# Kernel optimization log

Measured on AMD Instinct MI355X. Metric: run time of the kernel, lower is better.

The kernel has to match this reference:

```python
import jax, jax.numpy as jnp
import numpy as np

B, U, N0, N1, E, H = 8, 8192, 64, 64, 128, 8
S = N0 * N1


def setup_inputs() -> dict:
    key = jax.random.key(0)
    ks = jax.random.split(key, 9)
    # regular grid over [-1, 1]^2 (meshgrid, 'ij' indexing)
    c0 = jnp.linspace(-1.0, 1.0, N0)
    c1 = jnp.linspace(-1.0, 1.0, N1)
    g0, g1 = jnp.meshgrid(c0, c1, indexing='ij')
    xc_on_grid = jnp.broadcast_to(jnp.stack([g0, g1], -1), (B, N0, N1, 2))
    xc_off_grid = jax.random.uniform(ks[0], (B, U, 2), minval=-1.0, maxval=1.0)
    zc_off_grid = jax.random.normal(ks[1], (B, U, E))
    zc_on_grid = jax.random.normal(ks[2], (B, N0, N1, E))
    latents = jax.random.normal(ks[3], (N0, N1, E))
    fake_embedding = jax.random.normal(ks[4], (E,))
    sc = 1.0 / np.sqrt(E).astype(np.float32)
    Wq = jax.random.normal(ks[5], (E, E)) * sc
    Wk = jax.random.normal(ks[6], (E, E)) * sc
    Wv = jax.random.normal(ks[7], (E, E)) * sc
    Wo = jax.random.normal(ks[8], (E, E)) * sc
    return dict(xc_off_grid=xc_off_grid, xc_on_grid=xc_on_grid,
                zc_off_grid=zc_off_grid, zc_on_grid=zc_on_grid,
                latents=latents, fake_embedding=fake_embedding,
                Wq=Wq, Wk=Wk, Wv=Wv, Wo=Wo, used_modality=0)


def _nearest_idx(x, x_grid):
    # nearest cell on a regular grid, flattened row-major (k=1 of nearest_gridded_neighbours)
    n0, n1 = x_grid.shape[1], x_grid.shape[2]
    c0 = x_grid[:, :, 0, 0]   # [B, n0]
    c1 = x_grid[:, 0, :, 1]   # [B, n1]
    sp0 = (c0[:, 1] - c0[:, 0])[:, None]
    sp1 = (c1[:, 1] - c1[:, 0])[:, None]
    i0 = jnp.clip(jnp.round((x[..., 0] - c0[:, :1]) / sp0), 0, n0 - 1)
    i1 = jnp.clip(jnp.round((x[..., 1] - c1[:, :1]) / sp1), 0, n1 - 1)
    return (i0 * n1 + i1).astype(jnp.int32)


def _cumcount(nearest):
    # duplicate-count within each grid cell via linear-recurrence associative scan
    # (same math as the torch complex-log scan: x_t = a_t*x_{t-1} + b_t, a=b=same-flag)
    sort_idx = jnp.argsort(nearest, axis=1, stable=True)
    ns = jnp.take_along_axis(nearest, sort_idx, axis=1)
    same = (ns == jnp.roll(ns, 1, axis=1)).astype(jnp.float32)
    same = same.at[:, 0].set(0.0)

    def combine(c1, c2):
        a1, b1 = c1
        a2, b2 = c2
        return a1 * a2, a2 * b1 + b2

    _, cc = jax.lax.associative_scan(combine, (same, same), axis=1)
    unsort = jnp.argsort(sort_idx, axis=1, stable=True)
    return jnp.take_along_axis(jnp.round(cc), unsort, axis=1).astype(jnp.int32)


def _mhca(q, kv, mask, Wq, Wk, Wv, Wo):
    # q: [N,1,E], kv: [N,P,E], mask: [N,1,P] (True = attend)
    N, P, Ed = kv.shape
    dh = Ed // H
    qh = (q @ Wq).reshape(N, 1, H, dh).transpose(0, 2, 1, 3)
    kh = (kv @ Wk).reshape(N, P, H, dh).transpose(0, 2, 1, 3)
    vh = (kv @ Wv).reshape(N, P, H, dh).transpose(0, 2, 1, 3)
    scores = jnp.einsum('nhqd,nhkd->nhqk', qh, kh) / jnp.sqrt(jnp.asarray(dh, qh.dtype))
    scores = jnp.where(mask[:, None, :, :], scores, -jnp.inf)
    attn = jax.nn.softmax(scores, axis=-1)
    out = jnp.einsum('nhqk,nhkd->nhqd', attn, vh)
    return out.transpose(0, 2, 1, 3).reshape(N, 1, Ed) @ Wo


def reference(xc_off_grid, xc_on_grid, zc_off_grid, zc_on_grid, latents,
              fake_embedding, Wq, Wk, Wv, Wo, used_modality):
    # PseudoTokenGridEncoder.forward, no-coarsening branch, used_modality=OFF_GRID
    Bb, Uu, Ee = zc_off_grid.shape
    n0, n1 = xc_on_grid.shape[1], xc_on_grid.shape[2]
    Ss = n0 * n1
    nearest = _nearest_idx(xc_off_grid, xc_on_grid)         # [B, U]
    cumcount = _cumcount(nearest)                           # [B, U]
    max_patch = int(jnp.max(cumcount)) + 2                  # data-dependent (eager)
    rows = nearest.reshape(-1) + jnp.repeat(jnp.arange(Bb) * Ss, Uu)
    cols = cumcount.reshape(-1)
    grid_stacked = jnp.zeros((Bb * Ss, max_patch, Ee), zc_off_grid.dtype)
    grid_stacked = grid_stacked.at[rows, cols].set(zc_off_grid.reshape(Bb * Uu, Ee))
    grid_stacked = grid_stacked.at[:, -1].set(fake_embedding)  # OFF_GRID -> fake token
    valid = jnp.zeros((Bb * Ss, max_patch), bool)
    valid = valid.at[rows, cols].set(True).at[:, -1].set(True)
    latent_flat = jnp.broadcast_to(latents.reshape(1, Ss, Ee), (Bb, Ss, Ee)).reshape(Bb * Ss, 1, Ee)
    out = _mhca(latent_flat, grid_stacked, valid[:, None, :], Wq, Wk, Wv, Wo)
    z_grid = out.reshape(Bb, n0, n1, Ee)
    return xc_on_grid, z_grid
```

## Files before the change

### kernel.cpp

```cpp
#include <hip/hip_runtime.h>
#include <hip/hip_bf16.h>

#define NB 8
#define NU 8192
#define GN0 64
#define GN1 64
#define NS 4096
#define NE 128
#define NH 8
#define CAP 20
#define NPTS (NB * NU)
#define NCELL (NB * NS)
#define OUT0 (NB * GN0 * GN1 * 2)


typedef __attribute__((ext_vector_type(8))) short short8v;
typedef __attribute__((ext_vector_type(4))) float float4v;

static __device__ inline unsigned pk2(float a, float b) {
  __hip_bfloat16 x = __float2bfloat16(a), y = __float2bfloat16(b);
  return ((unsigned)*(unsigned short*)&y << 16) | *(unsigned short*)&x;
}
static __device__ inline float bfs(short v) {
  unsigned u = (unsigned)(unsigned short)v << 16;
  return __builtin_bit_cast(float, u);
}

__global__ __launch_bounds__(256) void setup_kernel(
    const float* __restrict__ xc_on, const float* __restrict__ fake,
    const float* __restrict__ Wk, const float* __restrict__ Wv,
    const float* __restrict__ Wo,
    float* __restrict__ out, int* __restrict__ counts,
    float* __restrict__ fakeKV, __hip_bfloat16* __restrict__ Wt,
    __hip_bfloat16* __restrict__ Wot) {
  int t = threadIdx.x;
  int blk = blockIdx.x;
  if (blk < 64) {
    int idx = blk * 256 + t;
    ((float4*)out)[idx] = ((const float4*)xc_on)[idx];
    if (idx < NCELL / 4) ((int4*)counts)[idx] = int4{0, 0, 0, 0};
    return;
  }
  if (blk == 64) {
    __shared__ float frow[NE];
    if (t < NE) frow[t] = fake[t];
    __syncthreads();
    int e = t & 127, half = t >> 7;
    const float* W = half ? Wv : Wk;
    float acc = 0.f;
    for (int j = 0; j < NE; ++j) acc += frow[j] * W[j * NE + e];
    fakeKV[half * NE + e] = acc;
    return;
  }
  {
    int flat = (blk - 65) * 256 + t;
    int j = flat >> 7, e = flat & 127;
    Wt[e * NE + j] = __float2bfloat16(Wv[flat]);
    Wt[(128 + e) * NE + j] = __float2bfloat16(Wk[flat]);
    Wot[e * NE + j] = __float2bfloat16(Wo[flat]);
  }
}

__global__ __launch_bounds__(256) void vgemm_qf_kernel(
    const float* __restrict__ z, const float* __restrict__ xc_off,
    const float* __restrict__ xc_on, const __hip_bfloat16* __restrict__ Wt,
    const float* __restrict__ latents, const float* __restrict__ Wq,
    int* __restrict__ counts, unsigned short* __restrict__ lists,
    __hip_bfloat16* __restrict__ Vb, __hip_bfloat16* __restrict__ Kb,
    float* __restrict__ qf) {
  __shared__ __hip_bfloat16 zb[64 * 136];
  int tid = threadIdx.x;
  if ((int)blockIdx.x >= 1024) {
    float* lrow = (float*)zb;
    int s0 = ((int)blockIdx.x - 1024) * 8;
    for (int i = tid; i < 8 * NE; i += 256)
      lrow[i] = latents[(size_t)s0 * NE + i];
    __syncthreads();
    for (int i = tid; i < 8 * NE; i += 256) {
      int sl = i >> 7, e = i & 127;
      float acc = 0.f;
      for (int j = 0; j < NE; ++j) acc += lrow[sl * NE + j] * Wq[j * NE + e];
      qf[(size_t)(s0 + sl) * NE + e] = acc;
    }
    return;
  }
  int blk = ((int)blockIdx.x & 7) * 128 + ((int)blockIdx.x >> 3);
  size_t row0 = (size_t)blk * 64;
  for (int n = 0; n < 8; ++n) {
    int flat = n * 1024 + tid * 4;
    int r = flat >> 7, c = flat & 127;
    float4 v = *(const float4*)&z[(row0 + r) * NE + c];
    uint2 u = {pk2(v.x, v.y), pk2(v.z, v.w)};
    *(uint2*)&zb[r * 136 + c] = u;
  }
  if (tid < 64) {
    int p = (int)row0 + tid;
    int b = p >> 13;
    const float* g = xc_on + (size_t)b * (GN0 * GN1 * 2);
    float c00 = g[0], c01 = g[GN1 * 2], c10 = g[1], c11 = g[3];
    float x0 = xc_off[(size_t)p * 2 + 0];
    float x1 = xc_off[(size_t)p * 2 + 1];
    float f0 = rintf((x0 - c00) / (c01 - c00));
    float f1 = rintf((x1 - c10) / (c11 - c10));
    int i0 = (int)fminf(fmaxf(f0, 0.f), 63.f);
    int i1 = (int)fminf(fmaxf(f1, 0.f), 63.f);
    int cell = b * NS + i0 * GN1 + i1;
    int pos = atomicAdd(&counts[cell], 1);
    if (pos < CAP) lists[cell * CAP + pos] = (unsigned short)p;
  }
  __syncthreads();
  int wid = tid >> 6, l = tid & 63;
  int lr = l & 15, lk = l >> 4;
  const short* zl = (const short*)zb;
  const short* Wg = (const short*)Wt;
  float4v acc[4][4] = {};
  short8v bfrag[4][4];
#pragma unroll
  for (int ct = 0; ct < 4; ++ct) {
    int col = wid * 64 + ct * 16 + lr;
#pragma unroll
    for (int ks = 0; ks < 4; ++ks)
      bfrag[ct][ks] = *(const short8v*)&Wg[col * NE + ks * 32 + lk * 8];
  }
#pragma unroll
  for (int ks = 0; ks < 4; ++ks)
#pragma unroll
    for (int st = 0; st < 4; ++st) {
      short8v a = *(const short8v*)&zl[(st * 16 + lr) * 136 + ks * 32 + lk * 8];
#pragma unroll
      for (int ct = 0; ct < 4; ++ct)
        acc[st][ct] = __builtin_amdgcn_mfma_f32_16x16x32_bf16(bfrag[ct][ks], a, acc[st][ct], 0, 0, 0);
    }
  __hip_bfloat16* dst = (wid < 2) ? Vb : Kb;
  int cb = (wid & 1) * 64;
#pragma unroll
  for (int st = 0; st < 4; ++st)
#pragma unroll
    for (int ct = 0; ct < 4; ++ct) {
      size_t point = row0 + st * 16 + lr;
      int ch = cb + ct * 16 + lk * 4;
      uint2 u = {pk2(acc[st][ct][0], acc[st][ct][1]),
                 pk2(acc[st][ct][2], acc[st][ct][3])};
      *(uint2*)&dst[point * NE + ch] = u;
    }
}

__global__ __launch_bounds__(256) void attn_wo_kernel(
    const __hip_bfloat16* __restrict__ Vb, const __hip_bfloat16* __restrict__ Kb,
    const float* __restrict__ qf, const float* __restrict__ fakeKV,
    const int* __restrict__ counts, const unsigned short* __restrict__ lists,
    const __hip_bfloat16* __restrict__ Wot, float* __restrict__ out) {
  __shared__ __hip_bfloat16 ob[16 * 136];
  __shared__ float sc[4][4][24][8];
  __shared__ unsigned short pl[4][4][24];
  int tid = threadIdx.x, w = tid >> 6, l = tid & 63;
  int g = l >> 4, i = l & 15;
  int blk = ((int)blockIdx.x & 7) * 256 + ((int)blockIdx.x >> 3);
  int row = w * 4 + g;
  int cell = blk * 16 + row;
  int s = cell & (NS - 1);
  int cnt = min(counts[cell], CAP);
  for (int t = i; t < cnt; t += 16)
    pl[w][g][t] = lists[cell * CAP + t];
  int d0 = i * 8;
  float4 qa = *(const float4*)&qf[(size_t)s * NE + d0];
  float4 qb = *(const float4*)&qf[(size_t)s * NE + d0 + 4];
  __builtin_amdgcn_wave_barrier();
  for (int t = 0; t < cnt; ++t) {
    int pid = pl[w][g][t];
    short8v kv = *(const short8v*)(const short*)(Kb + (size_t)pid * NE + d0);
    float p = qa.x * bfs(kv[0]) + qa.y * bfs(kv[1]) + qa.z * bfs(kv[2]) + qa.w * bfs(kv[3])
            + qb.x * bfs(kv[4]) + qb.y * bfs(kv[5]) + qb.z * bfs(kv[6]) + qb.w * bfs(kv[7]);
    p += __shfl_xor(p, 1);
    if ((i & 1) == 0) sc[w][g][t][i >> 1] = p * 0.25f;
  }
  {
    float4 fa = *(const float4*)&fakeKV[d0];
    float4 fb = *(const float4*)&fakeKV[d0 + 4];
    float p = qa.x * fa.x + qa.y * fa.y + qa.z * fa.z + qa.w * fa.w
            + qb.x * fb.x + qb.y * fb.y + qb.z * fb.z + qb.w * fb.w;
    p += __shfl_xor(p, 1);
    if ((i & 1) == 0) sc[w][g][cnt][i >> 1] = p * 0.25f;
  }
  __builtin_amdgcn_wave_barrier();
  if (i < 8) {
    int T = cnt + 1;
    float m = -1e30f;
    for (int t = 0; t < T; ++t) m = fmaxf(m, sc[w][g][t][i]);
    float sum = 0.f;
    for (int t = 0; t < T; ++t) {
      float e = __expf(sc[w][g][t][i] - m);
      sum += e;
      sc[w][g][t][i] = e;
    }
    float inv = 1.f / sum;
    for (int t = 0; t < T; ++t) sc[w][g][t][i] *= inv;
  }
  __builtin_amdgcn_wave_barrier();
  int h = i >> 1;
  float va[8] = {0.f, 0.f, 0.f, 0.f, 0.f, 0.f, 0.f, 0.f};
  for (int t = 0; t < cnt; ++t) {
    int pid = pl[w][g][t];
    short8v vv = *(const short8v*)(const short*)(Vb + (size_t)pid * NE + d0);
    float wt = sc[w][g][t][h];
#pragma unroll
    for (int j = 0; j < 8; ++j) va[j] += wt * bfs(vv[j]);
  }
  {
    float4 fa = *(const float4*)&fakeKV[NE + d0];
    float4 fb = *(const float4*)&fakeKV[NE + d0 + 4];
    float wt = sc[w][g][cnt][h];
    va[0] += wt * fa.x; va[1] += wt * fa.y; va[2] += wt * fa.z; va[3] += wt * fa.w;
    va[4] += wt * fb.x; va[5] += wt * fb.y; va[6] += wt * fb.z; va[7] += wt * fb.w;
  }
  {
    uint4 u = {pk2(va[0], va[1]), pk2(va[2], va[3]),
               pk2(va[4], va[5]), pk2(va[6], va[7])};
    *(uint4*)&ob[row * 136 + d0] = u;
  }
  __syncthreads();
  int lr = l & 15, lk = l >> 4;
  const short* ol = (const short*)ob;
  const short* Wg = (const short*)Wot;
  short8v afr[4];
#pragma unroll
  for (int ks = 0; ks < 4; ++ks)
    afr[ks] = *(const short8v*)&ol[lr * 136 + ks * 32 + lk * 8];
  float4v acc[2] = {};
#pragma unroll
  for (int ct = 0; ct < 2; ++ct) {
    int col = (w * 2 + ct) * 16 + lr;
#pragma unroll
    for (int ks = 0; ks < 4; ++ks) {
      short8v bfr = *(const short8v*)&Wg[col * NE + ks * 32 + lk * 8];
      acc[ct] = __builtin_amdgcn_mfma_f32_16x16x32_bf16(afr[ks], bfr, acc[ct], 0, 0, 0);
    }
  }
  float* base = out + (size_t)OUT0 + (size_t)blk * 16 * NE;
#pragma unroll
  for (int ct = 0; ct < 2; ++ct)
#pragma unroll
    for (int r = 0; r < 4; ++r) {
      int orow = lk * 4 + r;
      int col = (w * 2 + ct) * 16 + lr;
      base[(size_t)orow * NE + col] = acc[ct][r];
    }
}

extern "C" void kernel_launch(void* const* d_in, const int* in_sizes, int n_in,
                              void* d_out, int out_size, void* d_ws, size_t ws_size,
                              hipStream_t stream) {
  const float* xc_off  = (const float*)d_in[0];
  const float* xc_on   = (const float*)d_in[1];
  const float* zc_off  = (const float*)d_in[2];
  const float* latents = (const float*)d_in[4];
  const float* fake    = (const float*)d_in[5];
  const float* Wq      = (const float*)d_in[6];
  const float* Wk      = (const float*)d_in[7];
  const float* Wv      = (const float*)d_in[8];
  const float* Wo      = (const float*)d_in[9];
  float* out = (float*)d_out;

  char* ws = (char*)d_ws;
  int*            counts = (int*)(ws);
  unsigned short* lists  = (unsigned short*)(ws + 131072);
  float*          qf     = (float*)(ws + 1441792);
  float*          fakeKV = (float*)(ws + 3538944);
  __hip_bfloat16* Wt     = (__hip_bfloat16*)(ws + 3539968);
  __hip_bfloat16* Wot    = (__hip_bfloat16*)(ws + 3605504);
  __hip_bfloat16* Vb     = (__hip_bfloat16*)(ws + 3638272);
  __hip_bfloat16* Kb     = (__hip_bfloat16*)(ws + 20415488);

  hipLaunchKernelGGL(setup_kernel, dim3(129), dim3(256), 0, stream,
                     xc_on, fake, Wk, Wv, Wo, out, counts, fakeKV, Wt, Wot);
  hipLaunchKernelGGL(vgemm_qf_kernel, dim3(1536), dim3(256), 0, stream,
                     zc_off, xc_off, xc_on, Wt, latents, Wq,
                     counts, lists, Vb, Kb, qf);
  hipLaunchKernelGGL(attn_wo_kernel, dim3(NCELL / 16), dim3(256), 0, stream,
                     Vb, Kb, qf, fakeKV, counts, lists, Wot, out);
}
```

Measured before the change: 62.48 us.

## Load GEMM A-fragments directly from global, halve tile, reorder qf blocks first

```diff
diff --git a/kernel.cpp b/kernel.cpp
--- a/kernel.cpp
+++ b/kernel.cpp
@@ -68,11 +68,10 @@
     int* __restrict__ counts, unsigned short* __restrict__ lists,
     __hip_bfloat16* __restrict__ Vb, __hip_bfloat16* __restrict__ Kb,
     float* __restrict__ qf) {
-  __shared__ __hip_bfloat16 zb[64 * 136];
+  __shared__ float lrow[8 * NE];
   int tid = threadIdx.x;
-  if ((int)blockIdx.x >= 1024) {
-    float* lrow = (float*)zb;
-    int s0 = ((int)blockIdx.x - 1024) * 8;
+  if ((int)blockIdx.x < 512) {
+    int s0 = (int)blockIdx.x * 8;
     for (int i = tid; i < 8 * NE; i += 256)
       lrow[i] = latents[(size_t)s0 * NE + i];
     __syncthreads();
@@ -84,17 +83,11 @@
     }
     return;
   }
-  int blk = ((int)blockIdx.x & 7) * 128 + ((int)blockIdx.x >> 3);
-  size_t row0 = (size_t)blk * 64;
-  for (int n = 0; n < 8; ++n) {
-    int flat = n * 1024 + tid * 4;
-    int r = flat >> 7, c = flat & 127;
-    float4 v = *(const float4*)&z[(row0 + r) * NE + c];
-    uint2 u = {pk2(v.x, v.y), pk2(v.z, v.w)};
-    *(uint2*)&zb[r * 136 + c] = u;
-  }
-  if (tid < 64) {
-    int p = (int)row0 + tid;
+  int hw = (int)blockIdx.x - 512;
+  int blk = (hw & 7) * 256 + (hw >> 3);
+  size_t p0 = (size_t)blk * 32;
+  if (tid < 32) {
+    int p = (int)p0 + tid;
     int b = p >> 13;
     const float* g = xc_on + (size_t)b * (GN0 * GN1 * 2);
     float c00 = g[0], c01 = g[GN1 * 2], c10 = g[1], c11 = g[3];
@@ -108,36 +101,44 @@
     int pos = atomicAdd(&counts[cell], 1);
     if (pos < CAP) lists[cell * CAP + pos] = (unsigned short)p;
   }
-  __syncthreads();
-  int wid = tid >> 6, l = tid & 63;
+  int w = tid >> 6, l = tid & 63;
   int lr = l & 15, lk = l >> 4;
-  const short* zl = (const short*)zb;
+  short8v afr[2][4];
+#pragma unroll
+  for (int st = 0; st < 2; ++st)
+#pragma unroll
+    for (int ks = 0; ks < 4; ++ks) {
+      const float* src = &z[(p0 + st * 16 + lr) * NE + ks * 32 + lk * 8];
+      float4 x = *(const float4*)src;
+      float4 y = *(const float4*)(src + 4);
+      uint4 u = {pk2(x.x, x.y), pk2(x.z, x.w), pk2(y.x, y.y), pk2(y.z, y.w)};
+      afr[st][ks] = __builtin_bit_cast(short8v, u);
+    }
   const short* Wg = (const short*)Wt;
-  float4v acc[4][4] = {};
   short8v bfrag[4][4];
 #pragma unroll
   for (int ct = 0; ct < 4; ++ct) {
-    int col = wid * 64 + ct * 16 + lr;
+    int col = w * 64 + ct * 16 + lr;
 #pragma unroll
     for (int ks = 0; ks < 4; ++ks)
       bfrag[ct][ks] = *(const short8v*)&Wg[col * NE + ks * 32 + lk * 8];
   }
+  float4v acc[2][4] = {};
 #pragma unroll
   for (int ks = 0; ks < 4; ++ks)
 #pragma unroll
-    for (int st = 0; st < 4; ++st) {
-      short8v a = *(const short8v*)&zl[(st * 16 + lr) * 136 + ks * 32 + lk * 8];
+    for (int st = 0; st < 2; ++st)
 #pragma unroll
       for (int ct = 0; ct < 4; ++ct)
-        acc[st][ct] = __builtin_amdgcn_mfma_f32_16x16x32_bf16(bfrag[ct][ks], a, acc[st][ct], 0, 0, 0);
-    }
-  __hip_bfloat16* dst = (wid < 2) ? Vb : Kb;
-  int cb = (wid & 1) * 64;
-#pragma unroll
-  for (int st = 0; st < 4; ++st)
+        acc[st][ct] = __builtin_amdgcn_mfma_f32_16x16x32_bf16(
+            bfrag[ct][ks], afr[st][ks], acc[st][ct], 0, 0, 0);
+  __hip_bfloat16* dst = (w < 2) ? Vb : Kb;
+  int cb = (w & 1) * 64;
+#pragma unroll
+  for (int st = 0; st < 2; ++st)
 #pragma unroll
     for (int ct = 0; ct < 4; ++ct) {
-      size_t point = row0 + st * 16 + lr;
+      size_t point = p0 + st * 16 + lr;
       int ch = cb + ct * 16 + lk * 4;
       uint2 u = {pk2(acc[st][ct][0], acc[st][ct][1]),
                  pk2(acc[st][ct][2], acc[st][ct][3])};
@@ -273,7 +274,7 @@
 
   hipLaunchKernelGGL(setup_kernel, dim3(129), dim3(256), 0, stream,
                      xc_on, fake, Wk, Wv, Wo, out, counts, fakeKV, Wt, Wot);
-  hipLaunchKernelGGL(vgemm_qf_kernel, dim3(1536), dim3(256), 0, stream,
+  hipLaunchKernelGGL(vgemm_qf_kernel, dim3(2560), dim3(256), 0, stream,
                      zc_off, xc_off, xc_on, Wt, latents, Wq,
                      counts, lists, Vb, Kb, qf);
   hipLaunchKernelGGL(attn_wo_kernel, dim3(NCELL / 16), dim3(256), 0, stream,
```

Result: slower. 77.02 us (+23.3%).
